# Kernel optimization log

Measured on AMD Instinct MI355X. Metric: run time of the kernel, lower is better.

## Reference

```python
import jax, jax.numpy as jnp
import numpy as np

USER_SIZE = 100000
EMBED_DIM = 512
BATCH, SEQ = 16, 2048
N_NODES = BATCH * SEQ          # 32768, adj is [N_NODES, N_NODES]
NNZ = N_NODES * 32             # avg degree 32
LN_EPS = 1e-5


def setup_inputs() -> dict:
    key = jax.random.key(0)
    ks = jax.random.split(key, 6)
    user_ids = jax.random.randint(ks[0], (BATCH, SEQ), 0, USER_SIZE, dtype=jnp.int32)
    adj_row = jax.random.randint(ks[1], (NNZ,), 0, N_NODES, dtype=jnp.int32)
    adj_col = jax.random.randint(ks[2], (NNZ,), 0, N_NODES, dtype=jnp.int32)
    # normalized-adjacency-like positive values, scaled ~1/degree to keep outputs stable
    adj_vals = jax.random.uniform(ks[3], (NNZ,), dtype=jnp.float32) / 32.0
    embedding = jax.random.normal(ks[4], (USER_SIZE, EMBED_DIM), dtype=jnp.float32) * 0.02
    W = jax.random.normal(ks[5], (EMBED_DIM, EMBED_DIM), dtype=jnp.float32) * 0.05
    bias = jnp.zeros((EMBED_DIM,), dtype=jnp.float32)
    ln_gamma = jnp.ones((EMBED_DIM,), dtype=jnp.float32)
    ln_beta = jnp.zeros((EMBED_DIM,), dtype=jnp.float32)
    return {"user_ids": user_ids, "adj_row": adj_row, "adj_col": adj_col,
            "adj_vals": adj_vals, "embedding": embedding, "W": W, "bias": bias,
            "ln_gamma": ln_gamma, "ln_beta": ln_beta}


def reference(user_ids, adj_row, adj_col, adj_vals, embedding, W, bias, ln_gamma, ln_beta):
    # Embedding lookup: [B, S, D]
    x = embedding[user_ids]
    # GCN on flattened nodes: support = X @ W, then sparse adj @ support + bias
    flat = x.reshape(N_NODES, EMBED_DIM)
    support = flat @ W                                  # [N, D]
    msgs = adj_vals[:, None] * support[adj_col]          # [nnz, D]
    agg = jax.ops.segment_sum(msgs, adj_row, num_segments=N_NODES)  # sparse.mm
    out = (agg + bias).reshape(BATCH, SEQ, EMBED_DIM)
    # LayerNorm over last dim
    mu = jnp.mean(out, axis=-1, keepdims=True)
    var = jnp.var(out, axis=-1, keepdims=True)
    out = (out - mu) * jax.lax.rsqrt(var + LN_EPS) * ln_gamma + ln_beta
    # Dropout is identity in eval mode
    return out
```

## Files before the change

### kernel.cpp

```cpp
#include <hip/hip_runtime.h>

#define N_NODES 32768
#define EMBED   512
#define NNZ_TOT 1048576
#define LN_EPS  1e-5f

typedef __attribute__((ext_vector_type(8))) short bf16x8;
typedef __attribute__((ext_vector_type(4))) float f32x4;
typedef __attribute__((ext_vector_type(4))) unsigned int u32x4;

__device__ __forceinline__ unsigned short f2bf(float x) {
    unsigned int u = __float_as_uint(x);
    unsigned int r = u + 0x7fffu + ((u >> 16) & 1u);
    return (unsigned short)(r >> 16);
}
__device__ __forceinline__ unsigned int pk2(float a, float b) {
    return (unsigned int)f2bf(a) | ((unsigned int)f2bf(b) << 16);
}

__global__ void zero_ints(int* __restrict__ p, int n) {
    int i = blockIdx.x * blockDim.x + threadIdx.x;
    if (i < n) p[i] = 0;
}

__global__ __launch_bounds__(256) void wt_kernel(
    const float* __restrict__ W, unsigned short* __restrict__ Wt)
{
    __shared__ float tile[32][33];
    const int tx = threadIdx.x & 31, ty = threadIdx.x >> 5;
    const int kb = blockIdx.y * 32, nb = blockIdx.x * 32;
#pragma unroll
    for (int i = 0; i < 32; i += 8)
        tile[ty + i][tx] = W[(long)(kb + ty + i) * EMBED + nb + tx];
    __syncthreads();
#pragma unroll
    for (int i = 0; i < 32; i += 8)
        Wt[(long)(nb + ty + i) * EMBED + kb + tx] = f2bf(tile[tx][ty + i]);
}

__global__ __launch_bounds__(256) void gemm_mfma(
    const int* __restrict__ uids, const float* __restrict__ emb,
    const unsigned short* __restrict__ Wt, unsigned short* __restrict__ support)
{
    __shared__ unsigned short As[128][40];
    __shared__ unsigned short Bs[128][40];

    const int t  = threadIdx.x;
    const int m0 = blockIdx.y * 128;
    const int n0 = blockIdx.x * 128;

    const int wave = t >> 6;
    const int lane = t & 63;
    const int wm   = (wave & 1) * 64;
    const int wn   = (wave >> 1) * 64;
    const int l16  = lane & 15;
    const int quad = lane >> 4;

    const int srow  = t >> 1;
    const int shalf = (t & 1) * 16;
    const int uid   = uids[m0 + srow];
    const float* arow = emb + (long)uid * EMBED + shalf;
    const unsigned short* brow = Wt + (long)(n0 + srow) * EMBED + shalf;

    f32x4 acc[4][4] = {};

    for (int k0 = 0; k0 < EMBED; k0 += 32) {
        const float4* ap = (const float4*)(arow + k0);
        float4 v0 = ap[0], v1 = ap[1], v2 = ap[2], v3 = ap[3];
        u32x4 lo, hi;
        lo.x = pk2(v0.x, v0.y); lo.y = pk2(v0.z, v0.w);
        lo.z = pk2(v1.x, v1.y); lo.w = pk2(v1.z, v1.w);
        hi.x = pk2(v2.x, v2.y); hi.y = pk2(v2.z, v2.w);
        hi.z = pk2(v3.x, v3.y); hi.w = pk2(v3.z, v3.w);
        *(u32x4*)&As[srow][shalf]     = lo;
        *(u32x4*)&As[srow][shalf + 8] = hi;
        const u32x4* bp = (const u32x4*)(brow + k0);
        *(u32x4*)&Bs[srow][shalf]     = bp[0];
        *(u32x4*)&Bs[srow][shalf + 8] = bp[1];
        __syncthreads();

        bf16x8 af[4], bfr[4];
#pragma unroll
        for (int i = 0; i < 4; ++i)
            af[i] = *(const bf16x8*)&As[wm + i * 16 + l16][quad * 8];
#pragma unroll
        for (int j = 0; j < 4; ++j)
            bfr[j] = *(const bf16x8*)&Bs[wn + j * 16 + l16][quad * 8];
#pragma unroll
        for (int i = 0; i < 4; ++i)
#pragma unroll
            for (int j = 0; j < 4; ++j)
                acc[i][j] = __builtin_amdgcn_mfma_f32_16x16x32_bf16(af[i], bfr[j], acc[i][j], 0, 0, 0);
        __syncthreads();
    }

#pragma unroll
    for (int i = 0; i < 4; ++i) {
#pragma unroll
        for (int j = 0; j < 4; ++j) {
            const int col = n0 + wn + j * 16 + l16;
#pragma unroll
            for (int r = 0; r < 4; ++r) {
                const int row = m0 + wm + i * 16 + quad * 4 + r;
                support[(long)row * EMBED + col] = f2bf(acc[i][j][r]);
            }
        }
    }
}

__global__ void hist_kernel(const int* __restrict__ adj_row, int* __restrict__ counts) {
    int i = blockIdx.x * blockDim.x + threadIdx.x;
    if (i < NNZ_TOT) atomicAdd(&counts[adj_row[i]], 1);
}

__global__ __launch_bounds__(1024) void scan_kernel(
    const int* __restrict__ counts, int* __restrict__ row_start)
{
    __shared__ int ssum[1024];
    const int t = threadIdx.x;
    const int base = t * 32;
    int loc[32];
    int run = 0;
#pragma unroll
    for (int i = 0; i < 32; ++i) {
        int c = counts[base + i];
        loc[i] = run;
        run += c;
    }
    ssum[t] = run;
    __syncthreads();
    for (int off = 1; off < 1024; off <<= 1) {
        int v = (t >= off) ? ssum[t - off] : 0;
        __syncthreads();
        ssum[t] += v;
        __syncthreads();
    }
    int prefix = (t > 0) ? ssum[t - 1] : 0;
#pragma unroll
    for (int i = 0; i < 32; ++i) row_start[base + i] = prefix + loc[i];
    if (t == 1023) row_start[N_NODES] = ssum[1023];
}

__global__ void scatter_kernel(
    const int* __restrict__ adj_row, const int* __restrict__ adj_col,
    const float* __restrict__ adj_vals, const int* __restrict__ row_start,
    int* __restrict__ cursor, int2* __restrict__ sc)
{
    int i = blockIdx.x * blockDim.x + threadIdx.x;
    if (i < NNZ_TOT) {
        int r = adj_row[i];
        int pos = atomicAdd(&cursor[r], 1);
        sc[row_start[r] + pos] = make_int2(adj_col[i], __float_as_int(adj_vals[i]));
    }
}

__global__ __launch_bounds__(256) void agg_ln_v3(
    const int* __restrict__ row_start, const int2* __restrict__ sc,
    const unsigned short* __restrict__ support,
    const float* __restrict__ bias, const float* __restrict__ gamma,
    const float* __restrict__ beta, float* __restrict__ out)
{
    const int t = threadIdx.x;
    const int n = __builtin_amdgcn_readfirstlane((blockIdx.x << 2) + (t >> 6));
    const int l = t & 63;
    const int s = row_start[n];
    const int e = row_start[n + 1];

    const unsigned short* supp_l = support + l * 8;

    float acc[8] = {};
    for (int i = s; i < e; i += 8) {
        int   col[8];
        float val[8];
#pragma unroll
        for (int j = 0; j < 8; ++j) {
            const bool ok = (i + j) < e;
            int2 p = sc[ok ? (i + j) : s];
            col[j] = __builtin_amdgcn_readfirstlane(p.x);
            val[j] = __uint_as_float(
                (unsigned)__builtin_amdgcn_readfirstlane(ok ? p.y : 0));
        }
        u32x4 u[8];
#pragma unroll
        for (int j = 0; j < 8; ++j)
            u[j] = *(const u32x4*)(supp_l + col[j] * EMBED);
#pragma unroll
        for (int j = 0; j < 8; ++j) {
            const float v = val[j];
#pragma unroll
            for (int q = 0; q < 4; ++q) {
                unsigned int a = u[j][q];
                acc[2 * q]     = fmaf(v, __uint_as_float(a << 16), acc[2 * q]);
                acc[2 * q + 1] = fmaf(v, __uint_as_float(a & 0xffff0000u), acc[2 * q + 1]);
            }
        }
    }

    const int d = l * 8;
    const float4 b0 = *(const float4*)(bias + d);
    const float4 b1 = *(const float4*)(bias + d + 4);
    acc[0] += b0.x; acc[1] += b0.y; acc[2] += b0.z; acc[3] += b0.w;
    acc[4] += b1.x; acc[5] += b1.y; acc[6] += b1.z; acc[7] += b1.w;

    float s1 = 0.f, s2 = 0.f;
#pragma unroll
    for (int j = 0; j < 8; ++j) { s1 += acc[j]; s2 = fmaf(acc[j], acc[j], s2); }
#pragma unroll
    for (int off = 32; off > 0; off >>= 1) {
        s1 += __shfl_xor(s1, off, 64);
        s2 += __shfl_xor(s2, off, 64);
    }
    const float mean = s1 * (1.f / 512.f);
    const float var  = s2 * (1.f / 512.f) - mean * mean;
    const float rstd = rsqrtf(var + LN_EPS);

    const float4 g0  = *(const float4*)(gamma + d);
    const float4 g1  = *(const float4*)(gamma + d + 4);
    const float4 be0 = *(const float4*)(beta + d);
    const float4 be1 = *(const float4*)(beta + d + 4);
    float4 o0, o1;
    o0.x = (acc[0] - mean) * rstd * g0.x + be0.x;
    o0.y = (acc[1] - mean) * rstd * g0.y + be0.y;
    o0.z = (acc[2] - mean) * rstd * g0.z + be0.z;
    o0.w = (acc[3] - mean) * rstd * g0.w + be0.w;
    o1.x = (acc[4] - mean) * rstd * g1.x + be1.x;
    o1.y = (acc[5] - mean) * rstd * g1.y + be1.y;
    o1.z = (acc[6] - mean) * rstd * g1.z + be1.z;
    o1.w = (acc[7] - mean) * rstd * g1.w + be1.w;

    float* orow = out + (long)n * EMBED + d;
    *(float4*)orow       = o0;
    *(float4*)(orow + 4) = o1;
}

extern "C" void kernel_launch(void* const* d_in, const int* in_sizes, int n_in,
                              void* d_out, int out_size, void* d_ws, size_t ws_size,
                              hipStream_t stream)
{
    const int*   user_ids = (const int*)  d_in[0];
    const int*   adj_row  = (const int*)  d_in[1];
    const int*   adj_col  = (const int*)  d_in[2];
    const float* adj_vals = (const float*)d_in[3];
    const float* emb      = (const float*)d_in[4];
    const float* W        = (const float*)d_in[5];
    const float* bias     = (const float*)d_in[6];
    const float* gamma    = (const float*)d_in[7];
    const float* beta     = (const float*)d_in[8];
    float* out = (float*)d_out;

    char* ws = (char*)d_ws;
    size_t off = 0;
    unsigned short* support = (unsigned short*)(ws + off); off += (size_t)N_NODES * EMBED * 2;
    unsigned short* Wt      = (unsigned short*)(ws + off); off += (size_t)EMBED * EMBED * 2;
    int2*  sc        = (int2*) (ws + off); off += (size_t)NNZ_TOT * 8;
    int*   row_start = (int*)  (ws + off); off += (size_t)(N_NODES + 4) * 4;
    int*   counts    = (int*)  (ws + off); off += (size_t)N_NODES * 4;
    int*   cursor    = (int*)  (ws + off); off += (size_t)N_NODES * 4;
    (void)off; (void)ws_size; (void)in_sizes; (void)n_in; (void)out_size;

    zero_ints<<<(2 * N_NODES + 255) / 256, 256, 0, stream>>>(counts, 2 * N_NODES);

    wt_kernel<<<dim3(16, 16), 256, 0, stream>>>(W, Wt);

    gemm_mfma<<<dim3(EMBED / 128, N_NODES / 128), 256, 0, stream>>>(user_ids, emb, Wt, support);

    hist_kernel<<<NNZ_TOT / 256, 256, 0, stream>>>(adj_row, counts);
    scan_kernel<<<1, 1024, 0, stream>>>(counts, row_start);
    scatter_kernel<<<NNZ_TOT / 256, 256, 0, stream>>>(adj_row, adj_col, adj_vals,
                                                      row_start, cursor, sc);

    agg_ln_v3<<<N_NODES / 4, 256, 0, stream>>>(row_start, sc, support,
                                               bias, gamma, beta, out);
}
```

Measured before the change: 565.0 us.

## Split aggregation into column slices for L2 locality, then separate LayerNorm pass

Replaces the fused per-row aggregate+LayerNorm kernel with a column-sliced aggregation kernel. Each block handles a 64-column slice of the feature dimension for 64 rows, so concurrently running blocks share a smaller working set of the bf16 support matrix and gather it with better cache reuse. Results go to a new fp32 intermediate buffer, and a separate LayerNorm kernel reads it back. The trade-off is an extra 64MB write plus read, re-reading the CSR index stream once per slice, and narrower 4-byte gathers per lane.

```diff
diff --git a/kernel.cpp b/kernel.cpp
--- a/kernel.cpp
+++ b/kernel.cpp
@@ -7,6 +7,8 @@
 
 typedef __attribute__((ext_vector_type(8))) short bf16x8;
 typedef __attribute__((ext_vector_type(4))) float f32x4;
+typedef __attribute__((ext_vector_type(2))) float f32x2;
+typedef __attribute__((ext_vector_type(2))) int i32x2;
 typedef __attribute__((ext_vector_type(4))) unsigned int u32x4;
 
 __device__ __forceinline__ unsigned short f2bf(float x) {
@@ -154,57 +156,79 @@
     }
 }
 
-__global__ __launch_bounds__(256) void agg_ln_v3(
-    const int* __restrict__ row_start, const int2* __restrict__ sc,
+__global__ __launch_bounds__(256) void agg_slice(
+    const int* __restrict__ row_start, const int* __restrict__ sc,
     const unsigned short* __restrict__ support,
-    const float* __restrict__ bias, const float* __restrict__ gamma,
+    const float* __restrict__ bias, float* __restrict__ agg)
+{
+    const int slice = blockIdx.x & 7;
+    const int rb    = blockIdx.x >> 3;
+    const int w     = threadIdx.x >> 6;
+    const int l     = threadIdx.x & 63;
+    const int half  = l >> 5;
+    const int sl    = l & 31;
+    const int d     = slice * 64 + sl * 2;
+
+    const unsigned short* suppd = support + d;
+    const float b0 = bias[d];
+    const float b1 = bias[d + 1];
+
+#pragma unroll 1
+    for (int it = 0; it < 8; ++it) {
+        const int row = rb * 64 + it * 8 + w * 2 + half;
+        const int s = row_start[row];
+        const int e = row_start[row + 1];
+
+        float a0 = 0.f, a1 = 0.f;
+        int i = s;
+        for (; i + 3 < e; i += 4) {
+            i32x2 p0 = __builtin_nontemporal_load((const i32x2*)(sc + 2 * i));
+            i32x2 p1 = __builtin_nontemporal_load((const i32x2*)(sc + 2 * (i + 1)));
+            i32x2 p2 = __builtin_nontemporal_load((const i32x2*)(sc + 2 * (i + 2)));
+            i32x2 p3 = __builtin_nontemporal_load((const i32x2*)(sc + 2 * (i + 3)));
+            unsigned int g0 = *(const unsigned int*)(suppd + (long)p0.x * EMBED);
+            unsigned int g1 = *(const unsigned int*)(suppd + (long)p1.x * EMBED);
+            unsigned int g2 = *(const unsigned int*)(suppd + (long)p2.x * EMBED);
+            unsigned int g3 = *(const unsigned int*)(suppd + (long)p3.x * EMBED);
+            float v0 = __int_as_float(p0.y), v1 = __int_as_float(p1.y);
+            float v2 = __int_as_float(p2.y), v3 = __int_as_float(p3.y);
+            a0 = fmaf(v0, __uint_as_float(g0 << 16), a0);
+            a1 = fmaf(v0, __uint_as_float(g0 & 0xffff0000u), a1);
+            a0 = fmaf(v1, __uint_as_float(g1 << 16), a0);
+            a1 = fmaf(v1, __uint_as_float(g1 & 0xffff0000u), a1);
+            a0 = fmaf(v2, __uint_as_float(g2 << 16), a0);
+            a1 = fmaf(v2, __uint_as_float(g2 & 0xffff0000u), a1);
+            a0 = fmaf(v3, __uint_as_float(g3 << 16), a0);
+            a1 = fmaf(v3, __uint_as_float(g3 & 0xffff0000u), a1);
+        }
+        for (; i < e; ++i) {
+            i32x2 p0 = __builtin_nontemporal_load((const i32x2*)(sc + 2 * i));
+            unsigned int g0 = *(const unsigned int*)(suppd + (long)p0.x * EMBED);
+            float v0 = __int_as_float(p0.y);
+            a0 = fmaf(v0, __uint_as_float(g0 << 16), a0);
+            a1 = fmaf(v0, __uint_as_float(g0 & 0xffff0000u), a1);
+        }
+
+        f32x2 o; o.x = a0 + b0; o.y = a1 + b1;
+        __builtin_nontemporal_store(o, (f32x2*)(agg + (long)row * EMBED + d));
+    }
+}
+
+__global__ __launch_bounds__(256) void ln_kernel(
+    const float* __restrict__ agg, const float* __restrict__ gamma,
     const float* __restrict__ beta, float* __restrict__ out)
 {
-    const int t = threadIdx.x;
-    const int n = __builtin_amdgcn_readfirstlane((blockIdx.x << 2) + (t >> 6));
-    const int l = t & 63;
-    const int s = row_start[n];
-    const int e = row_start[n + 1];
-
-    const unsigned short* supp_l = support + l * 8;
-
-    float acc[8] = {};
-    for (int i = s; i < e; i += 8) {
-        int   col[8];
-        float val[8];
-#pragma unroll
-        for (int j = 0; j < 8; ++j) {
-            const bool ok = (i + j) < e;
-            int2 p = sc[ok ? (i + j) : s];
-            col[j] = __builtin_amdgcn_readfirstlane(p.x);
-            val[j] = __uint_as_float(
-                (unsigned)__builtin_amdgcn_readfirstlane(ok ? p.y : 0));
-        }
-        u32x4 u[8];
-#pragma unroll
-        for (int j = 0; j < 8; ++j)
-            u[j] = *(const u32x4*)(supp_l + col[j] * EMBED);
-#pragma unroll
-        for (int j = 0; j < 8; ++j) {
-            const float v = val[j];
-#pragma unroll
-            for (int q = 0; q < 4; ++q) {
-                unsigned int a = u[j][q];
-                acc[2 * q]     = fmaf(v, __uint_as_float(a << 16), acc[2 * q]);
-                acc[2 * q + 1] = fmaf(v, __uint_as_float(a & 0xffff0000u), acc[2 * q + 1]);
-            }
-        }
-    }
-
-    const int d = l * 8;
-    const float4 b0 = *(const float4*)(bias + d);
-    const float4 b1 = *(const float4*)(bias + d + 4);
-    acc[0] += b0.x; acc[1] += b0.y; acc[2] += b0.z; acc[3] += b0.w;
-    acc[4] += b1.x; acc[5] += b1.y; acc[6] += b1.z; acc[7] += b1.w;
-
-    float s1 = 0.f, s2 = 0.f;
-#pragma unroll
-    for (int j = 0; j < 8; ++j) { s1 += acc[j]; s2 = fmaf(acc[j], acc[j], s2); }
+    const int row = (blockIdx.x << 2) + (threadIdx.x >> 6);
+    const int l = threadIdx.x & 63;
+    const float* a = agg + (long)row * EMBED + l * 8;
+
+    f32x4 x0 = __builtin_nontemporal_load((const f32x4*)a);
+    f32x4 x1 = __builtin_nontemporal_load((const f32x4*)(a + 4));
+
+    float s1 = x0[0] + x0[1] + x0[2] + x0[3] + x1[0] + x1[1] + x1[2] + x1[3];
+    float s2 = 0.f;
+#pragma unroll
+    for (int j = 0; j < 4; ++j) { s2 = fmaf(x0[j], x0[j], s2); s2 = fmaf(x1[j], x1[j], s2); }
 #pragma unroll
     for (int off = 32; off > 0; off >>= 1) {
         s1 += __shfl_xor(s1, off, 64);
@@ -214,23 +238,21 @@
     const float var  = s2 * (1.f / 512.f) - mean * mean;
     const float rstd = rsqrtf(var + LN_EPS);
 
-    const float4 g0  = *(const float4*)(gamma + d);
-    const float4 g1  = *(const float4*)(gamma + d + 4);
-    const float4 be0 = *(const float4*)(beta + d);
-    const float4 be1 = *(const float4*)(beta + d + 4);
-    float4 o0, o1;
-    o0.x = (acc[0] - mean) * rstd * g0.x + be0.x;
-    o0.y = (acc[1] - mean) * rstd * g0.y + be0.y;
-    o0.z = (acc[2] - mean) * rstd * g0.z + be0.z;
-    o0.w = (acc[3] - mean) * rstd * g0.w + be0.w;
-    o1.x = (acc[4] - mean) * rstd * g1.x + be1.x;
-    o1.y = (acc[5] - mean) * rstd * g1.y + be1.y;
-    o1.z = (acc[6] - mean) * rstd * g1.z + be1.z;
-    o1.w = (acc[7] - mean) * rstd * g1.w + be1.w;
-
-    float* orow = out + (long)n * EMBED + d;
-    *(float4*)orow       = o0;
-    *(float4*)(orow + 4) = o1;
+    const int d = l * 8;
+    f32x4 g0 = *(const f32x4*)(gamma + d);
+    f32x4 g1 = *(const f32x4*)(gamma + d + 4);
+    f32x4 e0 = *(const f32x4*)(beta + d);
+    f32x4 e1 = *(const f32x4*)(beta + d + 4);
+
+    f32x4 o0, o1;
+#pragma unroll
+    for (int j = 0; j < 4; ++j) {
+        o0[j] = (x0[j] - mean) * rstd * g0[j] + e0[j];
+        o1[j] = (x1[j] - mean) * rstd * g1[j] + e1[j];
+    }
+    float* orow = out + (long)row * EMBED + d;
+    __builtin_nontemporal_store(o0, (f32x4*)orow);
+    __builtin_nontemporal_store(o1, (f32x4*)(orow + 4));
 }
 
 extern "C" void kernel_launch(void* const* d_in, const int* in_sizes, int n_in,
@@ -256,6 +278,7 @@
     int*   row_start = (int*)  (ws + off); off += (size_t)(N_NODES + 4) * 4;
     int*   counts    = (int*)  (ws + off); off += (size_t)N_NODES * 4;
     int*   cursor    = (int*)  (ws + off); off += (size_t)N_NODES * 4;
+    float* agg       = (float*)(ws + off); off += (size_t)N_NODES * EMBED * 4;
     (void)off; (void)ws_size; (void)in_sizes; (void)n_in; (void)out_size;
 
     zero_ints<<<(2 * N_NODES + 255) / 256, 256, 0, stream>>>(counts, 2 * N_NODES);
@@ -269,6 +292,7 @@
     scatter_kernel<<<NNZ_TOT / 256, 256, 0, stream>>>(adj_row, adj_col, adj_vals,
                                                       row_start, cursor, sc);
 
-    agg_ln_v3<<<N_NODES / 4, 256, 0, stream>>>(row_start, sc, support,
-                                               bias, gamma, beta, out);
-}
+    agg_slice<<<8 * (N_NODES / 64), 256, 0, stream>>>(row_start, (const int*)sc, support, bias, agg);
+
+    ln_kernel<<<N_NODES / 4, 256, 0, stream>>>(agg, gamma, beta, out);
+}
```

Result: slower. 703.5 us (+24.5%).
